# Kernel optimization log

Measured on AMD Instinct MI355X. Metric: run time of the kernel, lower is better.

Reference implementation:

```python
import jax, jax.numpy as jnp
import numpy as np

NUM_HEADS = 16

def setup_inputs() -> dict:
    key = jax.random.key(0)
    ks = jax.random.split(key, 9)
    B, S, D = 8, 1024, 1024
    scale = 1.0 / np.sqrt(D)
    return {
        "query": jax.random.normal(ks[0], (B, S, D), jnp.float32),
        "key": jax.random.normal(ks[1], (B, S, D), jnp.float32),
        "value": jax.random.normal(ks[2], (B, S, D), jnp.float32),
        "Wq": jax.random.normal(ks[3], (D, D), jnp.float32) * scale,
        "bq": jnp.zeros((D,), jnp.float32),
        "Wk": jax.random.normal(ks[4], (D, D), jnp.float32) * scale,
        "bk": jnp.zeros((D,), jnp.float32),
        "Wv": jax.random.normal(ks[5], (D, D), jnp.float32) * scale,
        "bv": jnp.zeros((D,), jnp.float32),
    }

def reference(query, key, value, Wq, bq, Wk, bk, Wv, bv):
    B, S, D = query.shape
    H = NUM_HEADS
    hd = D // H
    def proj(x, W, b):
        # [B, S, D] -> [B, H, S, hd]  (nn.Linear uses x @ W.T + b)
        return (x @ W.T + b).reshape(B, -1, H, hd).transpose(0, 2, 1, 3)
    q = proj(query, Wq, bq)
    k = proj(key, Wk, bk)
    v = proj(value, Wv, bv)
    scores = jnp.einsum('bhqd,bhkd->bhqk', q, k) / (hd ** 0.5)
    w = jax.nn.softmax(scores, axis=-1)
    # relu(tanh(.)) on non-negative softmax probs == tanh, but keep faithful
    w = jax.nn.relu(jnp.tanh(w))
    attn = jnp.einsum('bhqk,bhkd->bhqd', w, v)  # [B, H, Sq, hd]
    attn_output = attn.transpose(0, 2, 1, 3).reshape(B, -1, D)
    attn_output_weights = jnp.mean(w, axis=1)  # [B, Sq, Sk]
    return attn_output, attn_output_weights
```

## Files before the change

kernel.cpp:

```cpp
#include <hip/hip_runtime.h>
#include <hip/hip_bf16.h>

using bf16x8 = __attribute__((ext_vector_type(8))) short;
using f32x4  = __attribute__((ext_vector_type(4))) float;
typedef unsigned short u16;

__device__ __forceinline__ u16 f2bf(float f) {
  unsigned int u = __float_as_uint(f);
  u += 0x7FFFu + ((u >> 16) & 1u);
  return (u16)(u >> 16);
}

__device__ __forceinline__ u16 f2bf_fast(float f) {
  return (u16)((__float_as_uint(f) + 0x8000u) >> 16);
}

__device__ __forceinline__ float bf2f(u16 b) {
  return __uint_as_float(((unsigned int)b) << 16);
}

__device__ __forceinline__ f32x4 mfma16(bf16x8 a, bf16x8 b, f32x4 c) {
  return __builtin_amdgcn_mfma_f32_16x16x32_bf16(a, b, c, 0, 0, 0);
}

#define EXP2F(x) __builtin_amdgcn_exp2f(x)
#define LOG2F(x) __builtin_amdgcn_logf(x)

__device__ __forceinline__ float tanh2(float p) {
  float x2 = p * p;
  return p * fmaf(x2, -0.33333333f, 1.0f);
}

#define EXP2_SHIFT 11.54156f

#define GLL16(gp, lp) __builtin_amdgcn_global_load_lds( \
    (const __attribute__((address_space(1))) unsigned*)(gp), \
    (__attribute__((address_space(3))) unsigned*)(lp), 16, 0, 0)

__global__ __launch_bounds__(256) void cvtX_kernel(
    const float* __restrict__ x0, const float* __restrict__ x1,
    const float* __restrict__ x2, u16* __restrict__ d0,
    u16* __restrict__ d1, u16* __restrict__ d2) {
  const float* src = (blockIdx.y == 0) ? x0 : (blockIdx.y == 1) ? x1 : x2;
  u16* dst = (blockIdx.y == 0) ? d0 : (blockIdx.y == 1) ? d1 : d2;
  const int i = (blockIdx.x * 256 + threadIdx.x) * 8;
  float4 v0 = *reinterpret_cast<const float4*>(src + i);
  float4 v1 = *reinterpret_cast<const float4*>(src + i + 4);
  u16 o[8] = {f2bf(v0.x), f2bf(v0.y), f2bf(v0.z), f2bf(v0.w),
              f2bf(v1.x), f2bf(v1.y), f2bf(v1.z), f2bf(v1.w)};
  *reinterpret_cast<int4*>(dst + i) = *reinterpret_cast<int4*>(o);
}

__global__ __launch_bounds__(256) void cvtW_kernel(
    const float* __restrict__ w0, const float* __restrict__ w1,
    const float* __restrict__ w2, u16* __restrict__ dst) {
  const float* src = (blockIdx.y == 0) ? w0 : (blockIdx.y == 1) ? w1 : w2;
  u16* d = dst + (size_t)blockIdx.y * 1048576;
  const int i = (blockIdx.x * 256 + threadIdx.x) * 8;
  float4 v0 = *reinterpret_cast<const float4*>(src + i);
  float4 v1 = *reinterpret_cast<const float4*>(src + i + 4);
  u16 o[8] = {f2bf(v0.x), f2bf(v0.y), f2bf(v0.z), f2bf(v0.w),
              f2bf(v1.x), f2bf(v1.y), f2bf(v1.z), f2bf(v1.w)};
  *reinterpret_cast<int4*>(d + i) = *reinterpret_cast<int4*>(o);
}

__global__ __launch_bounds__(256) void proj_kernel(
    const u16* __restrict__ Xq, const u16* __restrict__ Xk,
    const u16* __restrict__ Xv, const u16* __restrict__ Wbf,
    const float* __restrict__ Bq, const float* __restrict__ Bk,
    const float* __restrict__ Bv,
    u16* __restrict__ Yq, u16* __restrict__ Yk, u16* __restrict__ Yv)
{
  const int mat = blockIdx.z;
  const u16* X  = (mat == 0) ? Xq : (mat == 1) ? Xk : Xv;
  const u16* W  = Wbf + (size_t)mat * 1048576;
  const float* Bi = (mat == 0) ? Bq : (mat == 1) ? Bk : Bv;
  u16* Y = (mat == 0) ? Yq : (mat == 1) ? Yk : Yv;
  const float scale = (mat == 0) ? 0.125f * 1.44269504f : 1.0f;

  __shared__ u16 As[2][64][32];
  __shared__ u16 Bs[2][128][32];

  const int tid  = threadIdx.x;
  const int lane = tid & 63;
  const int w    = tid >> 6;
  const int m0 = blockIdx.x * 64;
  const int n0 = blockIdx.y * 128;
  const int wm = (w >> 1) * 32;
  const int wn = (w & 1) * 64;
  const int fr = lane & 15;
  const int fg = lane >> 4;

  const int srow = lane >> 2;
  const int scol = (lane & 3) * 8;
  const u16* agp = X + (size_t)(m0 + w*16 + srow) * 1024 + scol;
  const u16* bgp = W + (size_t)(n0 + w*32 + srow) * 1024 + scol;

  f32x4 zero = {0.f, 0.f, 0.f, 0.f};
  f32x4 acc[2][4];
#pragma unroll
  for (int i = 0; i < 2; i++)
#pragma unroll
    for (int j = 0; j < 4; j++) acc[i][j] = zero;

#define STAGE(buf, kk)                                            \
  do {                                                            \
    GLL16(agp + (kk),            &As[buf][w*16     ][0]);         \
    GLL16(bgp + (kk),            &Bs[buf][w*32     ][0]);         \
    GLL16(bgp + (kk) + 16*1024,  &Bs[buf][w*32 + 16][0]);         \
  } while (0)

  STAGE(0, 0);
  __syncthreads();

  int cur = 0;
  for (int kt = 0; kt < 32; kt++) {
    if (kt < 31) STAGE(cur ^ 1, (kt + 1) * 32);

    bf16x8 af[2], bff[4];
#pragma unroll
    for (int i = 0; i < 2; i++)
      af[i]  = *reinterpret_cast<const bf16x8*>(&As[cur][wm + i*16 + fr][fg*8]);
#pragma unroll
    for (int j = 0; j < 4; j++)
      bff[j] = *reinterpret_cast<const bf16x8*>(&Bs[cur][wn + j*16 + fr][fg*8]);
#pragma unroll
    for (int i = 0; i < 2; i++)
#pragma unroll
      for (int j = 0; j < 4; j++)
        acc[i][j] = mfma16(af[i], bff[j], acc[i][j]);

    __syncthreads();
    cur ^= 1;
  }
#undef STAGE

#pragma unroll
  for (int j = 0; j < 4; j++) {
    const int n = n0 + wn + j*16 + fr;
    const float bias = Bi[n];
#pragma unroll
    for (int i = 0; i < 2; i++) {
      const int mbase = m0 + wm + i*16 + fg*4;
      if (mat == 2) {
        u16 pk[4];
#pragma unroll
        for (int r = 0; r < 4; r++) pk[r] = f2bf((acc[i][j][r] + bias) * scale);
        const int bidx = mbase >> 10;
        const int s = mbase & 1023;
        *reinterpret_cast<uint2*>(&Y[((size_t)(bidx * 1024 + n)) * 1024 + s]) =
            *reinterpret_cast<uint2*>(pk);
      } else {
#pragma unroll
        for (int r = 0; r < 4; r++) {
          Y[(size_t)(mbase + r) * 1024 + n] = f2bf((acc[i][j][r] + bias) * scale);
        }
      }
    }
  }
}

__global__ __launch_bounds__(256) void attn_out_kernel(
    const u16* __restrict__ Qbf, const u16* __restrict__ Kbf, const u16* __restrict__ Vt,
    float* __restrict__ outA, float* __restrict__ rcpZ)
{
  const int bid = blockIdx.x;
  const int xcd = bid & 7;
  const int wi  = bid >> 3;
  const int qt  = wi & 15;
  const int bh  = ((wi >> 4) << 3) | xcd;
  const int b   = bh >> 4;
  const int h   = bh & 15;

  const int tid  = threadIdx.x;
  const int lane = tid & 63;
  const int w    = tid >> 6;
  const int fr = lane & 15;
  const int fg = lane >> 4;

  __shared__ u16 Ks[2][32][88];
  __shared__ u16 Vts[2][64][40];
  __shared__ u16 Tl[4][16][40];

  const int qbase = qt * 64 + w * 16;

  const u16* qp = Qbf + ((size_t)(b * 1024 + qbase + fr)) * 1024 + h * 64 + fg * 8;
  const bf16x8 qf0 = *reinterpret_cast<const bf16x8*>(qp);
  const bf16x8 qf1 = *reinterpret_cast<const bf16x8*>(qp + 32);

  const int krow = tid >> 3;
  const int koff = (tid & 7) * 8;
  const u16* kp = Kbf + ((size_t)(b * 1024 + krow)) * 1024 + h * 64 + koff;

  const int vrow = tid >> 2;
  const int voff = (tid & 3) * 8;
  const u16* vp = Vt + ((size_t)((b * 16 + h) * 64 + vrow)) * 1024 + voff;

  f32x4 zero = {0.f, 0.f, 0.f, 0.f};
  float zacc[4] = {0.f, 0.f, 0.f, 0.f};
  f32x4 o1[4], o3[4];
#pragma unroll
  for (int e = 0; e < 4; e++) { o1[e] = zero; o3[e] = zero; }

  {
    int4 kv = *reinterpret_cast<const int4*>(kp);
    int4 vv = *reinterpret_cast<const int4*>(vp);
    *reinterpret_cast<int4*>(&Ks[0][krow][koff]) = kv;
    *reinterpret_cast<int4*>(&Vts[0][vrow][voff]) = vv;
  }
  __syncthreads();
  int cur = 0;
  for (int kt = 0; kt < 32; kt++) {
    int4 kvn, vvn;
    if (kt < 31) {
      kvn = *reinterpret_cast<const int4*>(kp + (size_t)(kt + 1) * 32 * 1024);
      vvn = *reinterpret_cast<const int4*>(vp + (kt + 1) * 32);
    }

    bf16x8 k0a = *reinterpret_cast<const bf16x8*>(&Ks[cur][fr][fg*8]);
    bf16x8 k0b = *reinterpret_cast<const bf16x8*>(&Ks[cur][fr][32 + fg*8]);
    bf16x8 k1a = *reinterpret_cast<const bf16x8*>(&Ks[cur][16 + fr][fg*8]);
    bf16x8 k1b = *reinterpret_cast<const bf16x8*>(&Ks[cur][16 + fr][32 + fg*8]);
    f32x4 s0 = zero, s1 = zero;
    s0 = mfma16(qf0, k0a, s0); s0 = mfma16(qf1, k0b, s0);
    s1 = mfma16(qf0, k1a, s1); s1 = mfma16(qf1, k1b, s1);

#pragma unroll
    for (int r = 0; r < 4; r++) {
      float e0 = EXP2F(s0[r] - EXP2_SHIFT);
      float e1 = EXP2F(s1[r] - EXP2_SHIFT);
      zacc[r] += e0 + e1;
      Tl[w][fg*4 + r][fr]       = f2bf_fast(e0);
      Tl[w][fg*4 + r][16 + fr]  = f2bf_fast(e1);
    }
    bf16x8 af = *reinterpret_cast<const bf16x8*>(&Tl[w][fr][fg*8]);
    bf16x8 af3;
#pragma unroll
    for (int j = 0; j < 8; j++) {
      float e = bf2f((u16)af[j]);
      af3[j] = (short)f2bf_fast(e * e * e);
    }
#pragma unroll
    for (int e = 0; e < 4; e++) {
      bf16x8 bv = *reinterpret_cast<const bf16x8*>(&Vts[cur][e*16 + fr][fg*8]);
      o1[e] = mfma16(af,  bv, o1[e]);
      o3[e] = mfma16(af3, bv, o3[e]);
    }

    if (kt < 31) {
      *reinterpret_cast<int4*>(&Ks[cur ^ 1][krow][koff]) = kvn;
      *reinterpret_cast<int4*>(&Vts[cur ^ 1][vrow][voff]) = vvn;
    }
    __syncthreads();
    cur ^= 1;
  }

#pragma unroll
  for (int r = 0; r < 4; r++) {
    float z = zacc[r];
    z += __shfl_xor(z, 1); z += __shfl_xor(z, 2);
    z += __shfl_xor(z, 4); z += __shfl_xor(z, 8);
    zacc[r] = z;
  }
  float rz[4], rz3[4];
#pragma unroll
  for (int r = 0; r < 4; r++) {
    rz[r] = 1.0f / zacc[r];
    rz3[r] = rz[r] * rz[r] * rz[r] * 0.33333333f;
  }
  if (fr == 0) {
#pragma unroll
    for (int r = 0; r < 4; r++)
      rcpZ[((size_t)(b * 16 + h)) * 1024 + qbase + fg * 4 + r] = rz[r];
  }
#pragma unroll
  for (int e = 0; e < 4; e++)
#pragma unroll
    for (int r = 0; r < 4; r++)
      outA[((size_t)(b * 1024 + qbase + fg*4 + r)) * 1024 + h * 64 + e*16 + fr] =
          rz[r] * o1[e][r] - rz3[r] * o3[e][r];
}

__global__ __launch_bounds__(256) void attn_w_kernel(
    const u16* __restrict__ Qbf, const u16* __restrict__ Kbf,
    const float* __restrict__ rcpZ, float* __restrict__ outW)
{
  const int bid = blockIdx.x;
  const int b   = bid & 7;
  const int wi  = bid >> 3;
  const int qt  = wi & 31;
  const int ks  = wi >> 5;
  const int tid  = threadIdx.x;
  const int lane = tid & 63;
  const int w    = tid >> 6;
  const int qi = w >> 1;
  const int ki = w & 1;
  const int fr = lane & 15;
  const int fg = lane >> 4;

  __shared__ u16 Ksh[2][128][72];
  __shared__ float statsL[16][32];

  {
    const int hh = tid >> 5, rr = tid & 31;
    float rzv0 = rcpZ[((size_t)(b * 16 + hh)) * 1024 + qt * 32 + rr];
    statsL[hh][rr] = LOG2F(rzv0) - EXP2_SHIFT;
    float rzv1 = rcpZ[((size_t)(b * 16 + hh + 8)) * 1024 + qt * 32 + rr];
    statsL[hh + 8][rr] = LOG2F(rzv1) - EXP2_SHIFT;
  }

  const int srow = tid >> 1;
  const int scol = (tid & 1) * 32;
  const u16* kgp = Kbf + ((size_t)(b * 1024 + ks * 128 + srow)) * 1024 + scol;

  const u16* qp = Qbf + ((size_t)(b * 1024 + qt * 32 + qi * 16 + fr)) * 1024 + fg * 8;

  f32x4 wsum[4];
#pragma unroll
  for (int kt = 0; kt < 4; kt++) wsum[kt] = f32x4{0.f, 0.f, 0.f, 0.f};

  {
#pragma unroll
    for (int j = 0; j < 4; j++)
      *reinterpret_cast<int4*>(&Ksh[0][srow][scol + j*8]) =
          *reinterpret_cast<const int4*>(kgp + j*8);
  }
  __syncthreads();

  int cur = 0;
  for (int h = 0; h < 16; h++) {
    int4 kn[4];
    if (h < 15) {
#pragma unroll
      for (int j = 0; j < 4; j++)
        kn[j] = *reinterpret_cast<const int4*>(kgp + (h + 1) * 64 + j*8);
    }

    bf16x8 a0 = *reinterpret_cast<const bf16x8*>(qp + h * 64);
    bf16x8 a1 = *reinterpret_cast<const bf16x8*>(qp + h * 64 + 32);
    float cl[4];
#pragma unroll
    for (int r = 0; r < 4; r++) cl[r] = statsL[h][qi*16 + fg*4 + r];

#pragma unroll
    for (int kt = 0; kt < 4; kt++) {
      const int krow = ki * 64 + kt * 16 + fr;
      bf16x8 b0 = *reinterpret_cast<const bf16x8*>(&Ksh[cur][krow][fg*8]);
      bf16x8 b1 = *reinterpret_cast<const bf16x8*>(&Ksh[cur][krow][32 + fg*8]);
      f32x4 s = {0.f, 0.f, 0.f, 0.f};
      s = mfma16(a0, b0, s);
      s = mfma16(a1, b1, s);
#pragma unroll
      for (int r = 0; r < 4; r++)
        wsum[kt][r] += tanh2(EXP2F(s[r] + cl[r]));
    }

    if (h < 15) {
#pragma unroll
      for (int j = 0; j < 4; j++)
        *reinterpret_cast<int4*>(&Ksh[cur ^ 1][srow][scol + j*8]) = kn[j];
    }
    __syncthreads();
    cur ^= 1;
  }

#pragma unroll
  for (int kt = 0; kt < 4; kt++)
#pragma unroll
    for (int r = 0; r < 4; r++)
      outW[((size_t)(b*1024 + qt*32 + qi*16 + fg*4 + r)) * 1024 + ks*128 + ki*64 + kt*16 + fr] =
          wsum[kt][r] * 0.0625f;
}

extern "C" void kernel_launch(void* const* d_in, const int* in_sizes, int n_in,
                              void* d_out, int out_size, void* d_ws, size_t ws_size,
                              hipStream_t stream) {
  const float* query = (const float*)d_in[0];
  const float* key_  = (const float*)d_in[1];
  const float* value = (const float*)d_in[2];
  const float* Wq = (const float*)d_in[3];
  const float* bq = (const float*)d_in[4];
  const float* Wk = (const float*)d_in[5];
  const float* bk = (const float*)d_in[6];
  const float* Wv = (const float*)d_in[7];
  const float* bv = (const float*)d_in[8];

  float* outA = (float*)d_out;
  float* outW = outA + 8388608;

  u16* Qbf = (u16*)d_ws;
  u16* Kbf = Qbf + 8388608;
  u16* Vt  = Kbf + 8388608;
  u16* Xq  = Vt + 8388608;
  u16* Xk  = Xq + 8388608;
  u16* Xv  = Xk + 8388608;
  u16* Wbf = Xv + 8388608;
  float* rcpZ = (float*)(Wbf + 3145728);

  cvtW_kernel<<<dim3(512, 3), 256, 0, stream>>>(Wq, Wk, Wv, Wbf);
  cvtX_kernel<<<dim3(4096, 3), 256, 0, stream>>>(query, key_, value, Xq, Xk, Xv);
  proj_kernel<<<dim3(128, 8, 3), 256, 0, stream>>>(
      Xq, Xk, Xv, Wbf, bq, bk, bv, Qbf, Kbf, Vt);
  attn_out_kernel<<<dim3(2048), dim3(256), 0, stream>>>(Qbf, Kbf, Vt, outA, rcpZ);
  attn_w_kernel<<<dim3(2048), dim3(256), 0, stream>>>(Qbf, Kbf, rcpZ, outW);
}
```

Baseline: 271.6 us.

## Fuse fp32-to-bf16 input conversion into projection GEMM A-tile loading

Removes the separate cvtX kernel and has the projection kernel read fp32 query/key/value directly. Each A tile is loaded into registers, converted to bf16 with a faster rounding, and written to padded LDS after the MFMAs, overlapping with the next iteration. This drops a full write and re-read of bf16 copies of the inputs. In exchange, the fp32 A data is re-read by every n-block, doubling its bytes per block, and loads now pass through registers instead of direct-to-LDS.

```diff
diff --git a/kernel.cpp b/kernel.cpp
--- a/kernel.cpp
+++ b/kernel.cpp
@@ -36,20 +36,6 @@
 #define GLL16(gp, lp) __builtin_amdgcn_global_load_lds( \
     (const __attribute__((address_space(1))) unsigned*)(gp), \
     (__attribute__((address_space(3))) unsigned*)(lp), 16, 0, 0)
-
-__global__ __launch_bounds__(256) void cvtX_kernel(
-    const float* __restrict__ x0, const float* __restrict__ x1,
-    const float* __restrict__ x2, u16* __restrict__ d0,
-    u16* __restrict__ d1, u16* __restrict__ d2) {
-  const float* src = (blockIdx.y == 0) ? x0 : (blockIdx.y == 1) ? x1 : x2;
-  u16* dst = (blockIdx.y == 0) ? d0 : (blockIdx.y == 1) ? d1 : d2;
-  const int i = (blockIdx.x * 256 + threadIdx.x) * 8;
-  float4 v0 = *reinterpret_cast<const float4*>(src + i);
-  float4 v1 = *reinterpret_cast<const float4*>(src + i + 4);
-  u16 o[8] = {f2bf(v0.x), f2bf(v0.y), f2bf(v0.z), f2bf(v0.w),
-              f2bf(v1.x), f2bf(v1.y), f2bf(v1.z), f2bf(v1.w)};
-  *reinterpret_cast<int4*>(dst + i) = *reinterpret_cast<int4*>(o);
-}
 
 __global__ __launch_bounds__(256) void cvtW_kernel(
     const float* __restrict__ w0, const float* __restrict__ w1,
@@ -65,20 +51,20 @@
 }
 
 __global__ __launch_bounds__(256) void proj_kernel(
-    const u16* __restrict__ Xq, const u16* __restrict__ Xk,
-    const u16* __restrict__ Xv, const u16* __restrict__ Wbf,
+    const float* __restrict__ Xq, const float* __restrict__ Xk,
+    const float* __restrict__ Xv, const u16* __restrict__ Wbf,
     const float* __restrict__ Bq, const float* __restrict__ Bk,
     const float* __restrict__ Bv,
     u16* __restrict__ Yq, u16* __restrict__ Yk, u16* __restrict__ Yv)
 {
   const int mat = blockIdx.z;
-  const u16* X  = (mat == 0) ? Xq : (mat == 1) ? Xk : Xv;
+  const float* X = (mat == 0) ? Xq : (mat == 1) ? Xk : Xv;
   const u16* W  = Wbf + (size_t)mat * 1048576;
   const float* Bi = (mat == 0) ? Bq : (mat == 1) ? Bk : Bv;
   u16* Y = (mat == 0) ? Yq : (mat == 1) ? Yk : Yv;
   const float scale = (mat == 0) ? 0.125f * 1.44269504f : 1.0f;
 
-  __shared__ u16 As[2][64][32];
+  __shared__ u16 As[2][64][40];
   __shared__ u16 Bs[2][128][32];
 
   const int tid  = threadIdx.x;
@@ -93,7 +79,7 @@
 
   const int srow = lane >> 2;
   const int scol = (lane & 3) * 8;
-  const u16* agp = X + (size_t)(m0 + w*16 + srow) * 1024 + scol;
+  const float* axp = X + (size_t)(m0 + w*16 + srow) * 1024 + scol;
   const u16* bgp = W + (size_t)(n0 + w*32 + srow) * 1024 + scol;
 
   f32x4 zero = {0.f, 0.f, 0.f, 0.f};
@@ -103,19 +89,38 @@
 #pragma unroll
     for (int j = 0; j < 4; j++) acc[i][j] = zero;
 
-#define STAGE(buf, kk)                                            \
+#define STAGE_B(buf, kk)                                          \
   do {                                                            \
-    GLL16(agp + (kk),            &As[buf][w*16     ][0]);         \
     GLL16(bgp + (kk),            &Bs[buf][w*32     ][0]);         \
     GLL16(bgp + (kk) + 16*1024,  &Bs[buf][w*32 + 16][0]);         \
   } while (0)
 
-  STAGE(0, 0);
+#define CVT_WRITE_A(buf, v0, v1)                                  \
+  do {                                                            \
+    u16 pk[8] = {f2bf_fast((v0).x), f2bf_fast((v0).y),            \
+                 f2bf_fast((v0).z), f2bf_fast((v0).w),            \
+                 f2bf_fast((v1).x), f2bf_fast((v1).y),            \
+                 f2bf_fast((v1).z), f2bf_fast((v1).w)};           \
+    *reinterpret_cast<int4*>(&As[buf][w*16 + srow][scol]) =       \
+        *reinterpret_cast<int4*>(pk);                             \
+  } while (0)
+
+  {
+    float4 a0 = *reinterpret_cast<const float4*>(axp);
+    float4 a1 = *reinterpret_cast<const float4*>(axp + 4);
+    STAGE_B(0, 0);
+    CVT_WRITE_A(0, a0, a1);
+  }
   __syncthreads();
 
   int cur = 0;
   for (int kt = 0; kt < 32; kt++) {
-    if (kt < 31) STAGE(cur ^ 1, (kt + 1) * 32);
+    float4 an0, an1;
+    if (kt < 31) {
+      an0 = *reinterpret_cast<const float4*>(axp + (kt + 1) * 32);
+      an1 = *reinterpret_cast<const float4*>(axp + (kt + 1) * 32 + 4);
+      STAGE_B(cur ^ 1, (kt + 1) * 32);
+    }
 
     bf16x8 af[2], bff[4];
 #pragma unroll
@@ -130,10 +135,13 @@
       for (int j = 0; j < 4; j++)
         acc[i][j] = mfma16(af[i], bff[j], acc[i][j]);
 
+    if (kt < 31) CVT_WRITE_A(cur ^ 1, an0, an1);
+
     __syncthreads();
     cur ^= 1;
   }
-#undef STAGE
+#undef STAGE_B
+#undef CVT_WRITE_A
 
 #pragma unroll
   for (int j = 0; j < 4; j++) {
@@ -391,16 +399,12 @@
   u16* Qbf = (u16*)d_ws;
   u16* Kbf = Qbf + 8388608;
   u16* Vt  = Kbf + 8388608;
-  u16* Xq  = Vt + 8388608;
-  u16* Xk  = Xq + 8388608;
-  u16* Xv  = Xk + 8388608;
-  u16* Wbf = Xv + 8388608;
+  u16* Wbf = Vt + 8388608;
   float* rcpZ = (float*)(Wbf + 3145728);
 
   cvtW_kernel<<<dim3(512, 3), 256, 0, stream>>>(Wq, Wk, Wv, Wbf);
-  cvtX_kernel<<<dim3(4096, 3), 256, 0, stream>>>(query, key_, value, Xq, Xk, Xv);
   proj_kernel<<<dim3(128, 8, 3), 256, 0, stream>>>(
-      Xq, Xk, Xv, Wbf, bq, bk, bv, Qbf, Kbf, Vt);
+      query, key_, value, Wbf, bq, bk, bv, Qbf, Kbf, Vt);
   attn_out_kernel<<<dim3(2048), dim3(256), 0, stream>>>(Qbf, Kbf, Vt, outA, rcpZ);
   attn_w_kernel<<<dim3(2048), dim3(256), 0, stream>>>(Qbf, Kbf, rcpZ, outW);
 }
```

Result: faster. 263.7 us (-2.9%).

## Fuse fp32-to-bf16 input conversion into projection GEMM staging

Applied to the files above, without the earlier changes.

Removes the separate cvtX kernel that converted query/key/value to bf16. The projection kernel now streams fp32 activations straight into a swizzled fp32 LDS tile and converts them to bf16 when building the MFMA fragments. This drops one kernel launch and a full write plus re-read of the bf16 copies of the activations. In exchange, the GEMM now reads fp32 inputs again for every N-tile (8x re-read of twice the bytes), uses more LDS, and uses truncation-style rounding instead of round-to-nearest-even.

```diff
diff --git a/kernel.cpp b/kernel.cpp
--- a/kernel.cpp
+++ b/kernel.cpp
@@ -36,20 +36,6 @@
 #define GLL16(gp, lp) __builtin_amdgcn_global_load_lds( \
     (const __attribute__((address_space(1))) unsigned*)(gp), \
     (__attribute__((address_space(3))) unsigned*)(lp), 16, 0, 0)
-
-__global__ __launch_bounds__(256) void cvtX_kernel(
-    const float* __restrict__ x0, const float* __restrict__ x1,
-    const float* __restrict__ x2, u16* __restrict__ d0,
-    u16* __restrict__ d1, u16* __restrict__ d2) {
-  const float* src = (blockIdx.y == 0) ? x0 : (blockIdx.y == 1) ? x1 : x2;
-  u16* dst = (blockIdx.y == 0) ? d0 : (blockIdx.y == 1) ? d1 : d2;
-  const int i = (blockIdx.x * 256 + threadIdx.x) * 8;
-  float4 v0 = *reinterpret_cast<const float4*>(src + i);
-  float4 v1 = *reinterpret_cast<const float4*>(src + i + 4);
-  u16 o[8] = {f2bf(v0.x), f2bf(v0.y), f2bf(v0.z), f2bf(v0.w),
-              f2bf(v1.x), f2bf(v1.y), f2bf(v1.z), f2bf(v1.w)};
-  *reinterpret_cast<int4*>(dst + i) = *reinterpret_cast<int4*>(o);
-}
 
 __global__ __launch_bounds__(256) void cvtW_kernel(
     const float* __restrict__ w0, const float* __restrict__ w1,
@@ -65,21 +51,21 @@
 }
 
 __global__ __launch_bounds__(256) void proj_kernel(
-    const u16* __restrict__ Xq, const u16* __restrict__ Xk,
-    const u16* __restrict__ Xv, const u16* __restrict__ Wbf,
+    const float* __restrict__ Xq, const float* __restrict__ Xk,
+    const float* __restrict__ Xv, const u16* __restrict__ Wbf,
     const float* __restrict__ Bq, const float* __restrict__ Bk,
     const float* __restrict__ Bv,
     u16* __restrict__ Yq, u16* __restrict__ Yk, u16* __restrict__ Yv)
 {
   const int mat = blockIdx.z;
-  const u16* X  = (mat == 0) ? Xq : (mat == 1) ? Xk : Xv;
+  const float* X = (mat == 0) ? Xq : (mat == 1) ? Xk : Xv;
   const u16* W  = Wbf + (size_t)mat * 1048576;
   const float* Bi = (mat == 0) ? Bq : (mat == 1) ? Bk : Bv;
   u16* Y = (mat == 0) ? Yq : (mat == 1) ? Yk : Yv;
   const float scale = (mat == 0) ? 0.125f * 1.44269504f : 1.0f;
 
-  __shared__ u16 As[2][64][32];
-  __shared__ u16 Bs[2][128][32];
+  __shared__ float As32[2][64][32];
+  __shared__ u16  Bs[2][128][32];
 
   const int tid  = threadIdx.x;
   const int lane = tid & 63;
@@ -91,10 +77,13 @@
   const int fr = lane & 15;
   const int fg = lane >> 4;
 
-  const int srow = lane >> 2;
-  const int scol = (lane & 3) * 8;
-  const u16* agp = X + (size_t)(m0 + w*16 + srow) * 1024 + scol;
-  const u16* bgp = W + (size_t)(n0 + w*32 + srow) * 1024 + scol;
+  const int arow = lane >> 3;
+  const int acol = ((lane & 7) * 4) ^ ((arow & 3) * 8);
+  const float* axp = X + (size_t)(m0 + w*16 + arow) * 1024 + acol;
+
+  const int brow = lane >> 2;
+  const int bcol = (lane & 3) * 8;
+  const u16* bgp = W + (size_t)(n0 + w*32 + brow) * 1024 + bcol;
 
   f32x4 zero = {0.f, 0.f, 0.f, 0.f};
   f32x4 acc[2][4];
@@ -105,7 +94,8 @@
 
 #define STAGE(buf, kk)                                            \
   do {                                                            \
-    GLL16(agp + (kk),            &As[buf][w*16     ][0]);         \
+    GLL16(axp + (kk),            &As32[buf][w*16    ][0]);        \
+    GLL16(axp + (kk) + 8*1024,   &As32[buf][w*16 + 8][0]);        \
     GLL16(bgp + (kk),            &Bs[buf][w*32     ][0]);         \
     GLL16(bgp + (kk) + 16*1024,  &Bs[buf][w*32 + 16][0]);         \
   } while (0)
@@ -119,8 +109,17 @@
 
     bf16x8 af[2], bff[4];
 #pragma unroll
-    for (int i = 0; i < 2; i++)
-      af[i]  = *reinterpret_cast<const bf16x8*>(&As[cur][wm + i*16 + fr][fg*8]);
+    for (int i = 0; i < 2; i++) {
+      const int row = wm + i*16 + fr;
+      const float* ap = &As32[cur][row][(fg ^ (fr & 3)) * 8];
+      float4 v0 = *reinterpret_cast<const float4*>(ap);
+      float4 v1 = *reinterpret_cast<const float4*>(ap + 4);
+      u16 pk[8] = {f2bf_fast(v0.x), f2bf_fast(v0.y),
+                   f2bf_fast(v0.z), f2bf_fast(v0.w),
+                   f2bf_fast(v1.x), f2bf_fast(v1.y),
+                   f2bf_fast(v1.z), f2bf_fast(v1.w)};
+      af[i] = *reinterpret_cast<bf16x8*>(pk);
+    }
 #pragma unroll
     for (int j = 0; j < 4; j++)
       bff[j] = *reinterpret_cast<const bf16x8*>(&Bs[cur][wn + j*16 + fr][fg*8]);
@@ -391,16 +390,12 @@
   u16* Qbf = (u16*)d_ws;
   u16* Kbf = Qbf + 8388608;
   u16* Vt  = Kbf + 8388608;
-  u16* Xq  = Vt + 8388608;
-  u16* Xk  = Xq + 8388608;
-  u16* Xv  = Xk + 8388608;
-  u16* Wbf = Xv + 8388608;
+  u16* Wbf = Vt + 8388608;
   float* rcpZ = (float*)(Wbf + 3145728);
 
   cvtW_kernel<<<dim3(512, 3), 256, 0, stream>>>(Wq, Wk, Wv, Wbf);
-  cvtX_kernel<<<dim3(4096, 3), 256, 0, stream>>>(query, key_, value, Xq, Xk, Xv);
   proj_kernel<<<dim3(128, 8, 3), 256, 0, stream>>>(
-      Xq, Xk, Xv, Wbf, bq, bk, bv, Qbf, Kbf, Vt);
+      query, key_, value, Wbf, bq, bk, bv, Qbf, Kbf, Vt);
   attn_out_kernel<<<dim3(2048), dim3(256), 0, stream>>>(Qbf, Kbf, Vt, outA, rcpZ);
   attn_w_kernel<<<dim3(2048), dim3(256), 0, stream>>>(Qbf, Kbf, rcpZ, outW);
 }
```

Result: faster. 265.5 us (-2.2%).
